# Optimization experiments

Measured on AMD Instinct MI355X. Metric: run time of the kernel, lower is better.

Reference implementation:

```python
import jax, jax.numpy as jnp
import numpy as np

H = 16        # num_heads
HID = 2048    # hidden_size
DK = 128
DV = 128


def setup_inputs() -> dict:
    key = jax.random.key(0)
    ks = jax.random.split(key, 8)
    B, S = 4, 2048
    x = jax.random.normal(ks[0], (B, S, HID), dtype=jnp.float32)
    q = jax.random.normal(ks[1], (B, S, H, DK), dtype=jnp.float32)
    k = jax.random.normal(ks[2], (B, S, H, DK), dtype=jnp.float32)
    v = jax.random.normal(ks[3], (B, S, H, DV), dtype=jnp.float32)
    scale = 1.0 / np.sqrt(HID)
    Wa = jax.random.normal(ks[4], (H, HID), dtype=jnp.float32) * scale
    Wb = jax.random.normal(ks[5], (H, HID), dtype=jnp.float32) * scale
    dt_bias = jnp.ones((H,), dtype=jnp.float32)
    A_log = jnp.log(jax.random.uniform(ks[6], (H,), dtype=jnp.float32, minval=1e-4, maxval=16.0))
    return {"x": x, "q": q, "k": k, "v": v, "Wa": Wa, "Wb": Wb,
            "dt_bias": dt_bias, "A_log": A_log}


def reference(x, q, k, v, Wa, Wb, dt_bias, A_log):
    # gates: alpha (log-space negative decay), beta (write strength), both (B,S,H)
    alpha = -jnp.exp(A_log) * jax.nn.softplus(jnp.einsum('bsd,hd->bsh', x, Wa) + dt_bias)
    beta = jnp.einsum('bsd,hd->bsh', x, Wb)
    decay = jnp.exp(alpha)  # (B,S,H), in (0,1)

    # seq-major for scan
    qs = jnp.swapaxes(q, 0, 1)      # (S,B,H,DK)
    ks_ = jnp.swapaxes(k, 0, 1)
    vs = jnp.swapaxes(v, 0, 1)      # (S,B,H,DV)
    gs = jnp.swapaxes(decay, 0, 1)  # (S,B,H)
    bs = jnp.swapaxes(beta, 0, 1)

    B = x.shape[0]
    state0 = jnp.zeros((B, H, DK, DV), dtype=jnp.float32)

    def step(state, inp):
        q_i, k_i, v_i, g_i, b_i = inp
        state = state * g_i[..., None, None]                       # decay
        v_old = jnp.einsum('bhk,bhkv->bhv', k_i, state)            # read old value
        diff = (v_i - v_old) * b_i[..., None]                      # gated delta
        state = state + k_i[..., None] * diff[:, :, None, :]       # rank-1 write
        out = jnp.einsum('bhk,bhkv->bhv', q_i, state)              # query read
        return state, out

    _, outs = jax.lax.scan(step, state0, (qs, ks_, vs, gs, bs))
    return jnp.swapaxes(outs, 0, 1)  # (B,S,H,DV)
```

## Files before the change

### kernel.cpp

```cpp
#include <hip/hip_runtime.h>
#include <math.h>

constexpr int B_ = 4;
constexpr int S_ = 2048;
constexpr int H_ = 16;
constexpr int HID_ = 2048;
constexpr int DK_ = 128;
constexpr int DV_ = 128;

constexpr int CH_ = 16;
constexpr int NC_ = 4;
constexpr int COLS_ = DV_ / NC_;
constexpr int NCHS_ = S_ / CH_;

template <int CTRL>
__device__ __forceinline__ float dpp_add(float x) {
  int y = __builtin_amdgcn_update_dpp(0, __float_as_int(x), CTRL, 0xF, 0xF, true);
  return x + __int_as_float(y);
}
__device__ __forceinline__ float sum16(float x) {
  x = dpp_add<0xB1>(x);
  x = dpp_add<0x4E>(x);
  x = dpp_add<0x141>(x);
  x = dpp_add<0x140>(x);
  return x;
}
__device__ __forceinline__ float swz_xor16(float x) {
  int y = __builtin_amdgcn_ds_swizzle(__float_as_int(x), 0x401F);
  return __int_as_float(y);
}

__global__ __launch_bounds__(256) void gates_kernel(
    const float* __restrict__ x, const float* __restrict__ Wa,
    const float* __restrict__ Wb, const float* __restrict__ dt_bias,
    const float* __restrict__ A_log, float* __restrict__ decay,
    float* __restrict__ beta) {
  const int r0 = blockIdx.x * 4;
  const int w = threadIdx.x >> 6;
  const int lane = threadIdx.x & 63;

  const float4* x4 = reinterpret_cast<const float4*>(x);
  const float4* wbase = reinterpret_cast<const float4*>(w < 2 ? Wa : Wb);
  const int h0 = (w & 1) * 8;

  float acc[4][8];
#pragma unroll
  for (int i = 0; i < 4; ++i)
#pragma unroll
    for (int j = 0; j < 8; ++j) acc[i][j] = 0.f;

  for (int m = 0; m < 8; ++m) {
    const int kk = m * 64 + lane;
    float4 xv[4], wv[8];
#pragma unroll
    for (int i = 0; i < 4; ++i) xv[i] = x4[(size_t)(r0 + i) * (HID_ / 4) + kk];
#pragma unroll
    for (int j = 0; j < 8; ++j) wv[j] = wbase[(size_t)(h0 + j) * (HID_ / 4) + kk];
#pragma unroll
    for (int i = 0; i < 4; ++i)
#pragma unroll
      for (int j = 0; j < 8; ++j) {
        acc[i][j] = fmaf(xv[i].x, wv[j].x, acc[i][j]);
        acc[i][j] = fmaf(xv[i].y, wv[j].y, acc[i][j]);
        acc[i][j] = fmaf(xv[i].z, wv[j].z, acc[i][j]);
        acc[i][j] = fmaf(xv[i].w, wv[j].w, acc[i][j]);
      }
  }

  float myval = 0.f;
#pragma unroll
  for (int i = 0; i < 4; ++i)
#pragma unroll
    for (int j = 0; j < 8; ++j) {
      float v = sum16(acc[i][j]);
      v += __shfl_xor(v, 16, 64);
      v += __shfl_xor(v, 32, 64);
      if (lane == i * 8 + j) myval = v;
    }
  if (lane < 32) {
    const int i = lane >> 3, j = lane & 7;
    const int h = h0 + j;
    const int row = r0 + i;
    if (w < 2) {
      const float za = myval + dt_bias[h];
      const float sp = (za > 20.f) ? za : log1pf(expf(za));
      decay[(size_t)row * H_ + h] = expf(-expf(A_log[h]) * sp);
    } else {
      beta[(size_t)row * H_ + h] = myval;
    }
  }
}

__global__ __launch_bounds__(512) void scan_kernel(
    const float* __restrict__ qg, const float* __restrict__ kg,
    const float* __restrict__ vg, const float* __restrict__ decay,
    const float* __restrict__ beta, float* __restrict__ outg) {
  const int c = blockIdx.x;
  const int h = blockIdx.y;
  const int b = blockIdx.z;
  const int tid = threadIdx.x;
  const int sub = tid & 15;
  const int col = tid >> 4;

  __shared__ __align__(16) float lk[CH_ * DK_];
  __shared__ __align__(16) float lq[CH_ * DK_];
  __shared__ __align__(16) float lv[CH_ * COLS_];
  __shared__ __align__(16) float lgbq[CH_ * 4];

  const float4* k4 = reinterpret_cast<const float4*>(kg);
  const float4* q4 = reinterpret_cast<const float4*>(qg);
  const float4* v4 = reinterpret_cast<const float4*>(vg);
  float4* lk4 = reinterpret_cast<float4*>(lk);
  float4* lq4 = reinterpret_cast<float4*>(lq);
  float4* lv4 = reinterpret_cast<float4*>(lv);

  const int u0 = tid >> 5, d4 = tid & 31;
  const int ph = (d4 & 1) * 16 + (d4 >> 1);

  float4 pk = {}, pq = {}, pv = {};
  float pg = 0.f, pb = 0.f;

  auto loadRegs = [&](int s0) {
    const size_t base = ((size_t)(b * S_ + s0 + u0) * H_ + h) * (DK_ / 4) + d4;
    pk = k4[base];
    pq = q4[base];
    if (tid < 128) {
      const int uu = tid >> 3, e = tid & 7;
      pv = v4[((size_t)(b * S_ + s0 + uu) * H_ + h) * (DV_ / 4) + c * (COLS_ / 4) + e];
    }
    if (tid >= 128 && tid < 128 + CH_)
      pg = decay[(size_t)(b * S_ + s0 + (tid - 128)) * H_ + h];
    if (tid >= 160 && tid < 160 + CH_)
      pb = beta[(size_t)(b * S_ + s0 + (tid - 160)) * H_ + h];
  };

  auto writeLDS = [&]() {
    lk4[u0 * 32 + ph] = pk;
    lq4[u0 * 32 + ph] = pq;
    if (tid < 128) {
      const int uu = tid >> 3, e = tid & 7;
      lv4[uu * (COLS_ / 4) + e] = pv;
    }
    if (tid >= 128 && tid < 128 + CH_) lgbq[(tid - 128) * 4 + 0] = pg;
    if (tid >= 160 && tid < 160 + CH_) lgbq[(tid - 160) * 4 + 1] = pb;
    float p = fmaf(pq.x, pk.x, fmaf(pq.y, pk.y, fmaf(pq.z, pk.z, pq.w * pk.w)));
    p = sum16(p);
    p += swz_xor16(p);
    if ((tid & 31) == 0) lgbq[u0 * 4 + 2] = p;
  };

  struct Frag {
    float4 k0, k1, q0, q1, gbq;
    float v;
  };
  auto loadFrag = [&](int u) {
    Frag f;
    f.k0 = lk4[u * 32 + sub];
    f.k1 = lk4[u * 32 + 16 + sub];
    f.q0 = lq4[u * 32 + sub];
    f.q1 = lq4[u * 32 + 16 + sub];
    f.v = lv[u * COLS_ + col];
    f.gbq = *reinterpret_cast<const float4*>(&lgbq[u * 4]);
    return f;
  };

  float st[8];
#pragma unroll
  for (int r = 0; r < 8; ++r) st[r] = 0.f;

  auto step = [&](const Frag& f, int u, int s0) {
    const float g = f.gbq.x, bt = f.gbq.y, qk = f.gbq.z;
    const float kr[8] = {f.k0.x, f.k0.y, f.k0.z, f.k0.w, f.k1.x, f.k1.y, f.k1.z, f.k1.w};
    const float qr[8] = {f.q0.x, f.q0.y, f.q0.z, f.q0.w, f.q1.x, f.q1.y, f.q1.z, f.q1.w};
    float vp = 0.f, op = 0.f;
#pragma unroll
    for (int r = 0; r < 8; ++r) {
      vp = fmaf(kr[r], st[r], vp);
      op = fmaf(qr[r], st[r], op);
    }
    vp = sum16(vp);
    op = sum16(op);
    const float dlt = (f.v - g * vp) * bt;
#pragma unroll
    for (int r = 0; r < 8; ++r) st[r] = fmaf(kr[r], dlt, st[r] * g);
    if (sub == 0) {
      __builtin_nontemporal_store(
          fmaf(qk, dlt, g * op),
          &outg[((size_t)(b * S_ + s0 + u) * H_ + h) * DV_ + c * COLS_ + col]);
    }
  };

  loadRegs(0);
  writeLDS();
  __syncthreads();

  for (int ci = 0; ci < NCHS_; ++ci) {
    const int s0 = ci * CH_;
    if (ci + 1 < NCHS_) loadRegs(s0 + CH_);

    Frag cur = loadFrag(0);
    for (int u = 0; u < CH_ - 1; ++u) {
      Frag nxt = loadFrag(u + 1);
      step(cur, u, s0);
      cur = nxt;
    }
    step(cur, CH_ - 1, s0);

    __syncthreads();
    if (ci + 1 < NCHS_) writeLDS();
    __syncthreads();
  }
}

extern "C" void kernel_launch(void* const* d_in, const int* in_sizes, int n_in,
                              void* d_out, int out_size, void* d_ws, size_t ws_size,
                              hipStream_t stream) {
  const float* x = (const float*)d_in[0];
  const float* q = (const float*)d_in[1];
  const float* k = (const float*)d_in[2];
  const float* v = (const float*)d_in[3];
  const float* Wa = (const float*)d_in[4];
  const float* Wb = (const float*)d_in[5];
  const float* dtb = (const float*)d_in[6];
  const float* Alog = (const float*)d_in[7];
  float* out = (float*)d_out;

  float* decay = (float*)d_ws;
  float* beta = decay + (size_t)B_ * S_ * H_;

  gates_kernel<<<B_ * S_ / 4, 256, 0, stream>>>(x, Wa, Wb, dtb, Alog, decay, beta);
  scan_kernel<<<dim3(NC_, H_, B_), 512, 0, stream>>>(q, k, v, decay, beta, out);
}
```

Baseline: 729.2 us.

## Replace per-step recurrence with chunked WY-style delta rule within each 16-token chunk

The scan kernel now handles each 16-token chunk in matrix form instead of stepping token by token. It builds the intra-chunk K·K^T and Q·K^T decay-weighted matrices from log-space alpha and reads the state once for all tokens. It then solves a small triangular system for the deltas, computes the outputs, and applies one batched state update per chunk. Outputs are staged in LDS and written as coalesced float4 stores. The gates kernel now emits alpha instead of exp(alpha). The serial dependency shrinks to a 16-step triangular solve, at the cost of extra LDS traffic, more barriers, and exp/sum16 work per chunk.

```diff
diff --git a/kernel.cpp b/kernel.cpp
--- a/kernel.cpp
+++ b/kernel.cpp
@@ -13,6 +13,9 @@
 constexpr int COLS_ = DV_ / NC_;
 constexpr int NCHS_ = S_ / CH_;
 
+constexpr int LKW4_ = 33;
+constexpr int LVW_ = 36;
+
 template <int CTRL>
 __device__ __forceinline__ float dpp_add(float x) {
   int y = __builtin_amdgcn_update_dpp(0, __float_as_int(x), CTRL, 0xF, 0xF, true);
@@ -25,15 +28,11 @@
   x = dpp_add<0x140>(x);
   return x;
 }
-__device__ __forceinline__ float swz_xor16(float x) {
-  int y = __builtin_amdgcn_ds_swizzle(__float_as_int(x), 0x401F);
-  return __int_as_float(y);
-}
 
 __global__ __launch_bounds__(256) void gates_kernel(
     const float* __restrict__ x, const float* __restrict__ Wa,
     const float* __restrict__ Wb, const float* __restrict__ dt_bias,
-    const float* __restrict__ A_log, float* __restrict__ decay,
+    const float* __restrict__ A_log, float* __restrict__ alpha,
     float* __restrict__ beta) {
   const int r0 = blockIdx.x * 4;
   const int w = threadIdx.x >> 6;
@@ -84,7 +83,7 @@
     if (w < 2) {
       const float za = myval + dt_bias[h];
       const float sp = (za > 20.f) ? za : log1pf(expf(za));
-      decay[(size_t)row * H_ + h] = expf(-expf(A_log[h]) * sp);
+      alpha[(size_t)row * H_ + h] = -expf(A_log[h]) * sp;
     } else {
       beta[(size_t)row * H_ + h] = myval;
     }
@@ -93,8 +92,8 @@
 
 __global__ __launch_bounds__(512) void scan_kernel(
     const float* __restrict__ qg, const float* __restrict__ kg,
-    const float* __restrict__ vg, const float* __restrict__ decay,
-    const float* __restrict__ beta, float* __restrict__ outg) {
+    const float* __restrict__ vg, const float* __restrict__ alphag,
+    const float* __restrict__ betag, float* __restrict__ outg) {
   const int c = blockIdx.x;
   const int h = blockIdx.y;
   const int b = blockIdx.z;
@@ -102,10 +101,14 @@
   const int sub = tid & 15;
   const int col = tid >> 4;
 
-  __shared__ __align__(16) float lk[CH_ * DK_];
-  __shared__ __align__(16) float lq[CH_ * DK_];
-  __shared__ __align__(16) float lv[CH_ * COLS_];
-  __shared__ __align__(16) float lgbq[CH_ * 4];
+  __shared__ __align__(16) float lk[CH_ * LKW4_ * 4];
+  __shared__ __align__(16) float lq[CH_ * LKW4_ * 4];
+  __shared__ __align__(16) float lv[CH_ * LVW_];
+  __shared__ float lab[CH_], lbt[CH_], lgt[CH_], lrr[CH_];
+  __shared__ float lA[CH_ * CH_];
+  __shared__ float lAttT[CH_ * CH_];
+  __shared__ __align__(16) float lD[CH_ * LVW_];
+  __shared__ __align__(16) float lo[CH_ * LVW_];
 
   const float4* k4 = reinterpret_cast<const float4*>(kg);
   const float4* q4 = reinterpret_cast<const float4*>(qg);
@@ -113,6 +116,7 @@
   float4* lk4 = reinterpret_cast<float4*>(lk);
   float4* lq4 = reinterpret_cast<float4*>(lq);
   float4* lv4 = reinterpret_cast<float4*>(lv);
+  const float4* lo4 = reinterpret_cast<const float4*>(lo);
 
   const int u0 = tid >> 5, d4 = tid & 31;
   const int ph = (d4 & 1) * 16 + (d4 >> 1);
@@ -129,66 +133,25 @@
       pv = v4[((size_t)(b * S_ + s0 + uu) * H_ + h) * (DV_ / 4) + c * (COLS_ / 4) + e];
     }
     if (tid >= 128 && tid < 128 + CH_)
-      pg = decay[(size_t)(b * S_ + s0 + (tid - 128)) * H_ + h];
+      pg = alphag[(size_t)(b * S_ + s0 + (tid - 128)) * H_ + h];
     if (tid >= 160 && tid < 160 + CH_)
-      pb = beta[(size_t)(b * S_ + s0 + (tid - 160)) * H_ + h];
+      pb = betag[(size_t)(b * S_ + s0 + (tid - 160)) * H_ + h];
   };
 
   auto writeLDS = [&]() {
-    lk4[u0 * 32 + ph] = pk;
-    lq4[u0 * 32 + ph] = pq;
+    lk4[u0 * LKW4_ + ph] = pk;
+    lq4[u0 * LKW4_ + ph] = pq;
     if (tid < 128) {
       const int uu = tid >> 3, e = tid & 7;
-      lv4[uu * (COLS_ / 4) + e] = pv;
-    }
-    if (tid >= 128 && tid < 128 + CH_) lgbq[(tid - 128) * 4 + 0] = pg;
-    if (tid >= 160 && tid < 160 + CH_) lgbq[(tid - 160) * 4 + 1] = pb;
-    float p = fmaf(pq.x, pk.x, fmaf(pq.y, pk.y, fmaf(pq.z, pk.z, pq.w * pk.w)));
-    p = sum16(p);
-    p += swz_xor16(p);
-    if ((tid & 31) == 0) lgbq[u0 * 4 + 2] = p;
+      lv4[uu * (LVW_ / 4) + e] = pv;
+    }
+    if (tid >= 128 && tid < 128 + CH_) lab[tid - 128] = pg;
+    if (tid >= 160 && tid < 160 + CH_) lbt[tid - 160] = pb;
   };
 
-  struct Frag {
-    float4 k0, k1, q0, q1, gbq;
-    float v;
-  };
-  auto loadFrag = [&](int u) {
-    Frag f;
-    f.k0 = lk4[u * 32 + sub];
-    f.k1 = lk4[u * 32 + 16 + sub];
-    f.q0 = lq4[u * 32 + sub];
-    f.q1 = lq4[u * 32 + 16 + sub];
-    f.v = lv[u * COLS_ + col];
-    f.gbq = *reinterpret_cast<const float4*>(&lgbq[u * 4]);
-    return f;
-  };
-
   float st[8];
 #pragma unroll
   for (int r = 0; r < 8; ++r) st[r] = 0.f;
-
-  auto step = [&](const Frag& f, int u, int s0) {
-    const float g = f.gbq.x, bt = f.gbq.y, qk = f.gbq.z;
-    const float kr[8] = {f.k0.x, f.k0.y, f.k0.z, f.k0.w, f.k1.x, f.k1.y, f.k1.z, f.k1.w};
-    const float qr[8] = {f.q0.x, f.q0.y, f.q0.z, f.q0.w, f.q1.x, f.q1.y, f.q1.z, f.q1.w};
-    float vp = 0.f, op = 0.f;
-#pragma unroll
-    for (int r = 0; r < 8; ++r) {
-      vp = fmaf(kr[r], st[r], vp);
-      op = fmaf(qr[r], st[r], op);
-    }
-    vp = sum16(vp);
-    op = sum16(op);
-    const float dlt = (f.v - g * vp) * bt;
-#pragma unroll
-    for (int r = 0; r < 8; ++r) st[r] = fmaf(kr[r], dlt, st[r] * g);
-    if (sub == 0) {
-      __builtin_nontemporal_store(
-          fmaf(qk, dlt, g * op),
-          &outg[((size_t)(b * S_ + s0 + u) * H_ + h) * DV_ + c * COLS_ + col]);
-    }
-  };
 
   loadRegs(0);
   writeLDS();
@@ -198,16 +161,108 @@
     const int s0 = ci * CH_;
     if (ci + 1 < NCHS_) loadRegs(s0 + CH_);
 
-    Frag cur = loadFrag(0);
-    for (int u = 0; u < CH_ - 1; ++u) {
-      Frag nxt = loadFrag(u + 1);
-      step(cur, u, s0);
-      cur = nxt;
-    }
-    step(cur, CH_ - 1, s0);
-
-    __syncthreads();
+    {
+      const int p = tid >> 1, half = tid & 1;
+      const int t = p >> 4, i = p & 15;
+      const float4* kt = &lk4[t * LKW4_ + half * 16];
+      const float4* ki = &lk4[i * LKW4_ + half * 16];
+      const float4* qt = &lq4[t * LKW4_ + half * 16];
+      float dp = 0.f, dq = 0.f;
+#pragma unroll
+      for (int e = 0; e < 16; ++e) {
+        const float4 a = kt[e], bb = ki[e], qq = qt[e];
+        dp = fmaf(a.x, bb.x, fmaf(a.y, bb.y, fmaf(a.z, bb.z, fmaf(a.w, bb.w, dp))));
+        dq = fmaf(qq.x, bb.x, fmaf(qq.y, bb.y, fmaf(qq.z, bb.z, fmaf(qq.w, bb.w, dq))));
+      }
+      dp += __shfl_xor(dp, 1, 64);
+      dq += __shfl_xor(dq, 1, 64);
+      float ld = 0.f;
+#pragma unroll
+      for (int j = 1; j < 16; ++j) {
+        const float aj = lab[j];
+        ld += (j > i && j <= t) ? aj : 0.f;
+      }
+      if (half == 0) {
+        const float r = expf(ld);
+        lA[t * 16 + i] = (i < t) ? r * lbt[t] * dp : 0.f;
+        lAttT[i * 16 + t] = (i <= t) ? r * dq : 0.f;
+        if (i == 0) lgt[t] = expf(ld + lab[0]);
+        if (t == 15) lrr[i] = r;
+      }
+    }
+
+    float ks_mine = 0.f, qs_mine = 0.f;
+#pragma unroll
+    for (int t = 0; t < CH_; ++t) {
+      const float4 ka = lk4[t * LKW4_ + sub], kb = lk4[t * LKW4_ + 16 + sub];
+      const float4 qa = lq4[t * LKW4_ + sub], qb = lq4[t * LKW4_ + 16 + sub];
+      float ks = 0.f, qs = 0.f;
+      ks = fmaf(ka.x, st[0], ks); ks = fmaf(ka.y, st[1], ks);
+      ks = fmaf(ka.z, st[2], ks); ks = fmaf(ka.w, st[3], ks);
+      ks = fmaf(kb.x, st[4], ks); ks = fmaf(kb.y, st[5], ks);
+      ks = fmaf(kb.z, st[6], ks); ks = fmaf(kb.w, st[7], ks);
+      qs = fmaf(qa.x, st[0], qs); qs = fmaf(qa.y, st[1], qs);
+      qs = fmaf(qa.z, st[2], qs); qs = fmaf(qa.w, st[3], qs);
+      qs = fmaf(qb.x, st[4], qs); qs = fmaf(qb.y, st[5], qs);
+      qs = fmaf(qb.z, st[6], qs); qs = fmaf(qb.w, st[7], qs);
+      ks = sum16(ks);
+      qs = sum16(qs);
+      if (sub == t) { ks_mine = ks; qs_mine = qs; }
+    }
+
+    __syncthreads();
+
+    {
+      float areg[CH_];
+#pragma unroll
+      for (int t = 0; t < CH_; ++t) areg[t] = lA[t * 16 + sub];
+      const float bmine = lbt[sub] * (lv[sub * LVW_ + col] - lgt[sub] * ks_mine);
+      float d = 0.f;
+#pragma unroll
+      for (int t = 0; t < CH_; ++t) {
+        const float s = sum16(areg[t] * d);
+        if (sub == t) d = bmine - s;
+      }
+      lD[sub * LVW_ + col] = d;
+    }
+
+    __syncthreads();
+
+    {
+      float dd[CH_], at[CH_];
+#pragma unroll
+      for (int i = 0; i < CH_; ++i) dd[i] = lD[i * LVW_ + col];
+#pragma unroll
+      for (int i = 0; i < CH_; ++i) at[i] = lAttT[i * 16 + sub];
+      float o = lgt[sub] * qs_mine;
+#pragma unroll
+      for (int i = 0; i < CH_; ++i) o = fmaf(at[i], dd[i], o);
+      lo[sub * LVW_ + col] = o;
+
+      const float g15 = lgt[15];
+#pragma unroll
+      for (int r = 0; r < 8; ++r) st[r] *= g15;
+#pragma unroll
+      for (int i = 0; i < CH_; ++i) {
+        const float e = lrr[i] * dd[i];
+        const float4 ka = lk4[i * LKW4_ + sub], kb = lk4[i * LKW4_ + 16 + sub];
+        st[0] = fmaf(ka.x, e, st[0]); st[1] = fmaf(ka.y, e, st[1]);
+        st[2] = fmaf(ka.z, e, st[2]); st[3] = fmaf(ka.w, e, st[3]);
+        st[4] = fmaf(kb.x, e, st[4]); st[5] = fmaf(kb.y, e, st[5]);
+        st[6] = fmaf(kb.z, e, st[6]); st[7] = fmaf(kb.w, e, st[7]);
+      }
+    }
+
+    __syncthreads();
+
+    if (tid < 128) {
+      const int t = tid >> 3, e = tid & 7;
+      *reinterpret_cast<float4*>(
+          &outg[((size_t)(b * S_ + s0 + t) * H_ + h) * DV_ + c * COLS_ + e * 4]) =
+          lo4[t * (LVW_ / 4) + e];
+    }
     if (ci + 1 < NCHS_) writeLDS();
+
     __syncthreads();
   }
 }
@@ -225,9 +280,9 @@
   const float* Alog = (const float*)d_in[7];
   float* out = (float*)d_out;
 
-  float* decay = (float*)d_ws;
-  float* beta = decay + (size_t)B_ * S_ * H_;
-
-  gates_kernel<<<B_ * S_ / 4, 256, 0, stream>>>(x, Wa, Wb, dtb, Alog, decay, beta);
-  scan_kernel<<<dim3(NC_, H_, B_), 512, 0, stream>>>(q, k, v, decay, beta, out);
-}
+  float* alpha = (float*)d_ws;
+  float* beta = alpha + (size_t)B_ * S_ * H_;
+
+  gates_kernel<<<B_ * S_ / 4, 256, 0, stream>>>(x, Wa, Wb, dtb, Alog, alpha, beta);
+  scan_kernel<<<dim3(NC_, H_, B_), 512, 0, stream>>>(q, k, v, alpha, beta, out);
+}
```

After: 955.7 us. 31.1% more time.

## Stage scan outputs in LDS for vectorized stores and remap block grid

Applied to the files above, without the earlier changes.

Scalar per-step output stores from sub==0 lanes are replaced by writes into an LDS buffer, which 128 threads then flush per chunk as 16-byte nontemporal stores. The inner step loop is fully unrolled with explicit double-buffered register fragments. The 3D grid becomes a 1D grid with a custom id-to-(c,h,b) mapping, likely to spread or group blocks across XCDs. This adds LDS use and a store phase between the chunk barriers.

```diff
diff --git a/kernel.cpp b/kernel.cpp
--- a/kernel.cpp
+++ b/kernel.cpp
@@ -12,6 +12,8 @@
 constexpr int NC_ = 4;
 constexpr int COLS_ = DV_ / NC_;
 constexpr int NCHS_ = S_ / CH_;
+
+typedef float f32x4_ __attribute__((ext_vector_type(4)));
 
 template <int CTRL>
 __device__ __forceinline__ float dpp_add(float x) {
@@ -94,10 +96,12 @@
 __global__ __launch_bounds__(512) void scan_kernel(
     const float* __restrict__ qg, const float* __restrict__ kg,
     const float* __restrict__ vg, const float* __restrict__ decay,
-    const float* __restrict__ beta, float* __restrict__ outg) {
-  const int c = blockIdx.x;
-  const int h = blockIdx.y;
-  const int b = blockIdx.z;
+    const float* __restrict__ betag, float* __restrict__ outg) {
+  const int id = blockIdx.x;
+  const int g_ = (id & 7) | ((id >> 5) << 3);
+  const int c = (id >> 3) & 3;
+  const int h = g_ & 15;
+  const int b = g_ >> 4;
   const int tid = threadIdx.x;
   const int sub = tid & 15;
   const int col = tid >> 4;
@@ -106,6 +110,7 @@
   __shared__ __align__(16) float lq[CH_ * DK_];
   __shared__ __align__(16) float lv[CH_ * COLS_];
   __shared__ __align__(16) float lgbq[CH_ * 4];
+  __shared__ __align__(16) float lo[CH_ * COLS_];
 
   const float4* k4 = reinterpret_cast<const float4*>(kg);
   const float4* q4 = reinterpret_cast<const float4*>(qg);
@@ -113,6 +118,7 @@
   float4* lk4 = reinterpret_cast<float4*>(lk);
   float4* lq4 = reinterpret_cast<float4*>(lq);
   float4* lv4 = reinterpret_cast<float4*>(lv);
+  const f32x4_* lo4n = reinterpret_cast<const f32x4_*>(lo);
 
   const int u0 = tid >> 5, d4 = tid & 31;
   const int ph = (d4 & 1) * 16 + (d4 >> 1);
@@ -131,7 +137,7 @@
     if (tid >= 128 && tid < 128 + CH_)
       pg = decay[(size_t)(b * S_ + s0 + (tid - 128)) * H_ + h];
     if (tid >= 160 && tid < 160 + CH_)
-      pb = beta[(size_t)(b * S_ + s0 + (tid - 160)) * H_ + h];
+      pb = betag[(size_t)(b * S_ + s0 + (tid - 160)) * H_ + h];
   };
 
   auto writeLDS = [&]() {
@@ -149,46 +155,12 @@
     if ((tid & 31) == 0) lgbq[u0 * 4 + 2] = p;
   };
 
-  struct Frag {
-    float4 k0, k1, q0, q1, gbq;
-    float v;
-  };
-  auto loadFrag = [&](int u) {
-    Frag f;
-    f.k0 = lk4[u * 32 + sub];
-    f.k1 = lk4[u * 32 + 16 + sub];
-    f.q0 = lq4[u * 32 + sub];
-    f.q1 = lq4[u * 32 + 16 + sub];
-    f.v = lv[u * COLS_ + col];
-    f.gbq = *reinterpret_cast<const float4*>(&lgbq[u * 4]);
-    return f;
-  };
-
   float st[8];
 #pragma unroll
   for (int r = 0; r < 8; ++r) st[r] = 0.f;
 
-  auto step = [&](const Frag& f, int u, int s0) {
-    const float g = f.gbq.x, bt = f.gbq.y, qk = f.gbq.z;
-    const float kr[8] = {f.k0.x, f.k0.y, f.k0.z, f.k0.w, f.k1.x, f.k1.y, f.k1.z, f.k1.w};
-    const float qr[8] = {f.q0.x, f.q0.y, f.q0.z, f.q0.w, f.q1.x, f.q1.y, f.q1.z, f.q1.w};
-    float vp = 0.f, op = 0.f;
-#pragma unroll
-    for (int r = 0; r < 8; ++r) {
-      vp = fmaf(kr[r], st[r], vp);
-      op = fmaf(qr[r], st[r], op);
-    }
-    vp = sum16(vp);
-    op = sum16(op);
-    const float dlt = (f.v - g * vp) * bt;
-#pragma unroll
-    for (int r = 0; r < 8; ++r) st[r] = fmaf(kr[r], dlt, st[r] * g);
-    if (sub == 0) {
-      __builtin_nontemporal_store(
-          fmaf(qk, dlt, g * op),
-          &outg[((size_t)(b * S_ + s0 + u) * H_ + h) * DV_ + c * COLS_ + col]);
-    }
-  };
+  float4 kA[2], kB[2], qA[2], qB[2], gq[2];
+  float fv[2];
 
   loadRegs(0);
   writeLDS();
@@ -198,16 +170,60 @@
     const int s0 = ci * CH_;
     if (ci + 1 < NCHS_) loadRegs(s0 + CH_);
 
-    Frag cur = loadFrag(0);
-    for (int u = 0; u < CH_ - 1; ++u) {
-      Frag nxt = loadFrag(u + 1);
-      step(cur, u, s0);
-      cur = nxt;
-    }
-    step(cur, CH_ - 1, s0);
+    kA[0] = lk4[0 * 32 + sub];
+    kB[0] = lk4[0 * 32 + 16 + sub];
+    qA[0] = lq4[0 * 32 + sub];
+    qB[0] = lq4[0 * 32 + 16 + sub];
+    fv[0] = lv[0 * COLS_ + col];
+    gq[0] = *reinterpret_cast<const float4*>(&lgbq[0]);
+
+#pragma unroll
+    for (int u = 0; u < CH_; ++u) {
+      const int p = u & 1;
+      if (u + 1 < CH_) {
+        const int n = p ^ 1;
+        kA[n] = lk4[(u + 1) * 32 + sub];
+        kB[n] = lk4[(u + 1) * 32 + 16 + sub];
+        qA[n] = lq4[(u + 1) * 32 + sub];
+        qB[n] = lq4[(u + 1) * 32 + 16 + sub];
+        fv[n] = lv[(u + 1) * COLS_ + col];
+        gq[n] = *reinterpret_cast<const float4*>(&lgbq[(u + 1) * 4]);
+      }
+      const float gg = gq[p].x, bt = gq[p].y, qk = gq[p].z;
+      float vp = kA[p].x * st[0];
+      float op = qA[p].x * st[0];
+      vp = fmaf(kA[p].y, st[1], vp); op = fmaf(qA[p].y, st[1], op);
+      vp = fmaf(kA[p].z, st[2], vp); op = fmaf(qA[p].z, st[2], op);
+      vp = fmaf(kA[p].w, st[3], vp); op = fmaf(qA[p].w, st[3], op);
+      vp = fmaf(kB[p].x, st[4], vp); op = fmaf(qB[p].x, st[4], op);
+      vp = fmaf(kB[p].y, st[5], vp); op = fmaf(qB[p].y, st[5], op);
+      vp = fmaf(kB[p].z, st[6], vp); op = fmaf(qB[p].z, st[6], op);
+      vp = fmaf(kB[p].w, st[7], vp); op = fmaf(qB[p].w, st[7], op);
+      vp = sum16(vp);
+      op = sum16(op);
+      const float dlt = (fv[p] - gg * vp) * bt;
+      st[0] = fmaf(kA[p].x, dlt, st[0] * gg);
+      st[1] = fmaf(kA[p].y, dlt, st[1] * gg);
+      st[2] = fmaf(kA[p].z, dlt, st[2] * gg);
+      st[3] = fmaf(kA[p].w, dlt, st[3] * gg);
+      st[4] = fmaf(kB[p].x, dlt, st[4] * gg);
+      st[5] = fmaf(kB[p].y, dlt, st[5] * gg);
+      st[6] = fmaf(kB[p].z, dlt, st[6] * gg);
+      st[7] = fmaf(kB[p].w, dlt, st[7] * gg);
+      if (sub == 0) lo[u * COLS_ + col] = fmaf(qk, dlt, gg * op);
+    }
 
     __syncthreads();
+
+    if (tid < 128) {
+      const int t = tid >> 3, e = tid & 7;
+      __builtin_nontemporal_store(
+          lo4n[t * (COLS_ / 4) + e],
+          reinterpret_cast<f32x4_*>(
+              &outg[((size_t)(b * S_ + s0 + t) * H_ + h) * DV_ + c * COLS_ + e * 4]));
+    }
     if (ci + 1 < NCHS_) writeLDS();
+
     __syncthreads();
   }
 }
@@ -229,5 +245,5 @@
   float* beta = decay + (size_t)B_ * S_ * H_;
 
   gates_kernel<<<B_ * S_ / 4, 256, 0, stream>>>(x, Wa, Wb, dtb, Alog, decay, beta);
-  scan_kernel<<<dim3(NC_, H_, B_), 512, 0, stream>>>(q, k, v, decay, beta, out);
-}
+  scan_kernel<<<256, 512, 0, stream>>>(q, k, v, decay, beta, out);
+}
```

Measured after the change: 608.7 us. 16.5% less time.
